# Optimization experiments

Measured on AMD Instinct MI355X. Metric: run time of the kernel, lower is better.

## Reference

```python
import jax, jax.numpy as jnp
import numpy as np

H = 16          # n_heads
DH = 128        # head_dim
DR = 64         # rope_dim
DC = DH - DR    # content_dim = 64
THETA = 10000.0
SCALE = 1.0 / np.sqrt(DH)


def _rope_tables(T, dtype):
    inv = 1.0 / (THETA ** (jnp.arange(0, DR, 2, dtype=jnp.float32) / DR))  # [DR/2]
    t = jnp.arange(T, dtype=jnp.float32)
    freqs = jnp.outer(t, inv)  # [T, DR/2]
    return jnp.cos(freqs).astype(dtype), jnp.sin(freqs).astype(dtype)


def _apply_rope(x, cos, sin):
    # x: [B,H,T,DR]; cos/sin: [T,DR/2] broadcast over B,H
    d = x.shape[-1] // 2
    x1, x2 = x[..., :d], x[..., d:]
    return jnp.concatenate([x1 * cos - x2 * sin, x1 * sin + x2 * cos], axis=-1)


def setup_inputs() -> dict:
    key = jax.random.key(0)
    ks = jax.random.split(key, 9)
    B, T, D = 1, 2048, 2048
    s = 0.02
    return {
        "x": jax.random.normal(ks[0], (B, T, D), jnp.float32),
        "Wq_down": jax.random.normal(ks[1], (D, 512), jnp.float32) * s,
        "Wq_up": jax.random.normal(ks[2], (512, H * DC), jnp.float32) * s,
        "Wq_rope": jax.random.normal(ks[3], (D, H * DR), jnp.float32) * s,
        "Wkv_down": jax.random.normal(ks[4], (D, 512), jnp.float32) * s,
        "Wk_up": jax.random.normal(ks[5], (512, H * DC), jnp.float32) * s,
        "Wv_up": jax.random.normal(ks[6], (512, H * DH), jnp.float32) * s,
        "Wk_rope": jax.random.normal(ks[7], (D, H * DR), jnp.float32) * s,
        "Wo": jax.random.normal(ks[8], (H * DH, D), jnp.float32) * s,
    }


def reference(x, Wq_down, Wq_up, Wq_rope, Wkv_down, Wk_up, Wv_up, Wk_rope, Wo):
    B, T, D = x.shape
    # low-rank query path: down then up, content part only
    q_content = ((x @ Wq_down) @ Wq_up).reshape(B, T, H, DC).transpose(0, 2, 1, 3)
    q_pos = (x @ Wq_rope).reshape(B, T, H, DR).transpose(0, 2, 1, 3)
    kv_latent = x @ Wkv_down                    # [B,T,d_latent]
    k_pos = (x @ Wk_rope).reshape(B, T, H, DR).transpose(0, 2, 1, 3)

    cos, sin = _rope_tables(T, x.dtype)
    q_pos = _apply_rope(q_pos, cos, sin)
    k_pos = _apply_rope(k_pos, cos, sin)

    k_content = (kv_latent @ Wk_up).reshape(B, T, H, DC).transpose(0, 2, 1, 3)
    v = (kv_latent @ Wv_up).reshape(B, T, H, DH).transpose(0, 2, 1, 3)

    q = jnp.concatenate([q_content, q_pos], axis=-1)  # [B,H,T,DH]
    k = jnp.concatenate([k_content, k_pos], axis=-1)  # [B,H,T,DH]

    scores = jnp.einsum("bhtd,bhsd->bhts", q, k) * SCALE
    causal = jnp.tril(jnp.ones((T, T), dtype=bool))
    scores = jnp.where(causal, scores, jnp.finfo(scores.dtype).min)
    attn = jax.nn.softmax(scores, axis=-1)
    out = jnp.einsum("bhts,bhsd->bhtd", attn, v)       # [B,H,T,DH]
    out = out.transpose(0, 2, 1, 3).reshape(B, T, H * DH)
    return out @ Wo
```

## Files before the change

### kernel.cpp

```cpp
#include <hip/hip_runtime.h>
#include <math.h>

#define T_SEQ 2048
#define D_MODEL 2048
#define H_HEADS 16
#define DH 128
#define DR 64
#define DC 64
#define D_LAT 512
#define SEGLEN 7
#define NSEG_TOT 46
#define NSEG_OF(q) ((2 * (q) + 2 + SEGLEN - 1) / SEGLEN)
#define QSCALE (0.08838834764831845f * 1.4426950408889634f)

typedef __attribute__((ext_vector_type(8))) short short8;
typedef __attribute__((ext_vector_type(4))) short short4v;
typedef __attribute__((ext_vector_type(4))) float f32x4;

#if __has_builtin(__builtin_amdgcn_exp2f)
#define EXP2(x) __builtin_amdgcn_exp2f(x)
#else
#define EXP2(x) exp2f(x)
#endif

__device__ __forceinline__ float bf2f(short b) {
    unsigned u = ((unsigned)(unsigned short)b) << 16;
    return __builtin_bit_cast(float, u);
}
__device__ __forceinline__ short f2bf(float f) {
    unsigned u = __builtin_bit_cast(unsigned, f);
    unsigned r = u + 0x7fffu + ((u >> 16) & 1u);
    return (short)(r >> 16);
}
__device__ __forceinline__ unsigned f2bf_tru(float f) {
    return __builtin_bit_cast(unsigned, f) >> 16;
}

#define GLD_LDS(gp, lp) \
    __builtin_amdgcn_global_load_lds( \
        (const __attribute__((address_space(1))) void*)(gp), \
        (__attribute__((address_space(3))) void*)(lp), 16, 0, 0)

__device__ __forceinline__ void ct_tile(float (*tile)[33],
                                        const float* __restrict__ W,
                                        short* __restrict__ Wt,
                                        int R, int C, int ldo, int rel) {
    int bx = rel % (C / 32), by = rel / (C / 32);
    int c0 = bx * 32, r0 = by * 32;
    int tx = threadIdx.x & 31, ty = threadIdx.x >> 5;
    #pragma unroll
    for (int i = 0; i < 4; ++i)
        tile[ty + i * 8][tx] = W[(size_t)(r0 + ty + i * 8) * C + c0 + tx];
    __syncthreads();
    #pragma unroll
    for (int i = 0; i < 4; ++i)
        Wt[(size_t)(c0 + ty + i * 8) * ldo + r0 + tx] = f2bf(tile[tx][ty + i * 8]);
    __syncthreads();
}

__global__ __launch_bounds__(256) void prep(const float* __restrict__ x,
                                            short* __restrict__ xb,
                                            const float* __restrict__ Wqd,
                                            const float* __restrict__ Wkvd,
                                            const float* __restrict__ Wqr,
                                            const float* __restrict__ Wkr,
                                            const float* __restrict__ Wqu,
                                            const float* __restrict__ Wku,
                                            const float* __restrict__ Wvu,
                                            const float* __restrict__ Wo,
                                            short* __restrict__ WdT,
                                            short* __restrict__ WupT2,
                                            short* __restrict__ WoT) {
    __shared__ float tile[32][33];
    int bid = blockIdx.x;
    if (bid < 4096) {
        int i = bid * 1024 + threadIdx.x * 4;
        float4 f = *(const float4*)&x[i];
        short4v o;
        o.x = f2bf(f.x); o.y = f2bf(f.y); o.z = f2bf(f.z); o.w = f2bf(f.w);
        *(short4v*)&xb[i] = o;
    } else if (bid < 5120) {
        ct_tile(tile, Wqd,  WdT + (size_t)0 * 2048,    2048, 512,  2048, bid - 4096);
    } else if (bid < 6144) {
        ct_tile(tile, Wkvd, WdT + (size_t)512 * 2048,  2048, 512,  2048, bid - 5120);
    } else if (bid < 8192) {
        ct_tile(tile, Wqr,  WdT + (size_t)1024 * 2048, 2048, 1024, 2048, bid - 6144);
    } else if (bid < 10240) {
        ct_tile(tile, Wkr,  WdT + (size_t)2048 * 2048, 2048, 1024, 2048, bid - 8192);
    } else if (bid < 10752) {
        ct_tile(tile, Wqu,  WupT2 + (size_t)0 * 512,    512, 1024, 512, bid - 10240);
    } else if (bid < 11264) {
        ct_tile(tile, Wku,  WupT2 + (size_t)1024 * 512, 512, 1024, 512, bid - 10752);
    } else if (bid < 12288) {
        ct_tile(tile, Wvu,  WupT2 + (size_t)2048 * 512, 512, 2048, 512, bid - 11264);
    } else {
        ct_tile(tile, Wo,   WoT, 2048, 2048, 2048, bid - 12288);
    }
}

__global__ __launch_bounds__(256) void transpose_bf16(const short* __restrict__ in,
                                                      short* __restrict__ vTc,
                                                      int ldi) {
    __shared__ short tile[64][65];
    int c0 = blockIdx.x * 64, t0 = blockIdx.y * 64;
    int tx = threadIdx.x & 31, ty = threadIdx.x >> 5;
    #pragma unroll
    for (int i = 0; i < 8; ++i) {
        int r = ty + i * 8;
        int vv = *(const int*)&in[(size_t)(t0 + r) * ldi + c0 + tx * 2];
        tile[r][tx * 2]     = (short)(vv & 0xffff);
        tile[r][tx * 2 + 1] = (short)(((unsigned)vv) >> 16);
    }
    __syncthreads();
    #pragma unroll
    for (int i = 0; i < 8; ++i) {
        int G = i * 256 + threadIdx.x;
        int ch2 = G >> 10;
        int rem = G & 1023;
        int dl = rem >> 4;
        int mp = rem & 15;
        int dval = c0 + dl;
        int h = dval >> 7, d128 = dval & 127;
        int kl = 4 * ((mp >> 2) ^ (d128 & 3)) + (mp & 3);
        unsigned lo = (unsigned short)tile[ch2 * 32 + kl][dl];
        unsigned hi = (unsigned short)tile[ch2 * 32 + kl + 16][dl];
        int chg = (t0 >> 5) + ch2;
        size_t off = ((size_t)(h * 64 + chg)) * 4096 + d128 * 32 + mp * 2;
        *(int*)&vTc[off] = (int)(lo | (hi << 16));
    }
}

__global__ __launch_bounds__(256) void gemm_bt(const short* __restrict__ A,
                                               const short* __restrict__ A2,
                                               const short* __restrict__ Bt,
                                               short* __restrict__ C0,
                                               short* __restrict__ C1,
                                               short* __restrict__ C2,
                                               short* __restrict__ C3,
                                               int N, int Kblk,
                                               int lda, int ldb, int ldc,
                                               int ncut, int scut, float cscale) {
    __shared__ short As[128 * 64];
    __shared__ short Bs[128 * 64];
    const int tid = threadIdx.x;
    const int wave = tid >> 6, lane = tid & 63;
    const int lin = blockIdx.x;
    const int X = N >> 7, Xq = X >> 2;
    const int xcd = lin & 7;
    int r = lin >> 3;
    const int bx = (xcd & 3) * Xq + (r % Xq); r /= Xq;
    const int by = (xcd >> 2) * 8 + (r & 7);
    const int bz = r >> 3;
    const int row0 = by * 128, col0 = bx * 128;
    const int kbase = bz * Kblk;
    const short* Ause = (col0 < ncut) ? A : A2;
    short* Cuse = (bz == 0) ? C0 : (bz == 1) ? C1 : (bz == 2) ? C2 : C3;
    const int wr = (wave >> 1) * 64, wc = (wave & 1) * 64;
    const int lr = lane & 15, quad = lane >> 4;

    f32x4 acc[4][4];
    #pragma unroll
    for (int i = 0; i < 4; ++i)
        #pragma unroll
        for (int j = 0; j < 4; ++j) acc[i][j] = (f32x4){0.f, 0.f, 0.f, 0.f};

    for (int k0 = kbase; k0 < kbase + Kblk; k0 += 64) {
        __syncthreads();
        #pragma unroll
        for (int it = 0; it < 4; ++it) {
            int idx = wave * 64 + it * 256 + lane;
            int row = idx >> 3;
            int scg = (idx & 7) ^ (row & 7);
            const short* ga = Ause + (size_t)(row0 + row) * lda + k0 + scg * 8;
            const short* gb = Bt   + (size_t)(col0 + row) * ldb + k0 + scg * 8;
            int lds0 = (wave * 64 + it * 256) * 8;
            GLD_LDS(ga, &As[lds0]);
            GLD_LDS(gb, &Bs[lds0]);
        }
        __syncthreads();

        #pragma unroll
        for (int kk = 0; kk < 2; ++kk) {
            short8 af[4], bfr[4];
            #pragma unroll
            for (int i = 0; i < 4; ++i)
                af[i] = *(const short8*)
                    &As[(wr + i * 16 + lr) * 64 + (((kk * 4 + quad) ^ (lr & 7)) * 8)];
            #pragma unroll
            for (int j = 0; j < 4; ++j)
                bfr[j] = *(const short8*)
                    &Bs[(wc + j * 16 + lr) * 64 + (((kk * 4 + quad) ^ (lr & 7)) * 8)];
            #pragma unroll
            for (int i = 0; i < 4; ++i)
                #pragma unroll
                for (int j = 0; j < 4; ++j)
                    acc[i][j] = __builtin_amdgcn_mfma_f32_16x16x32_bf16(
                        af[i], bfr[j], acc[i][j], 0, 0, 0);
        }
    }

    const float sc = (col0 < scut) ? cscale : 1.0f;
    #pragma unroll
    for (int i = 0; i < 4; ++i) {
        int rb = row0 + wr + i * 16 + quad * 4;
        #pragma unroll
        for (int j = 0; j < 4; ++j) {
            int c = col0 + wc + j * 16 + lr;
            #pragma unroll
            for (int rr = 0; rr < 4; ++rr)
                Cuse[(size_t)(rb + rr) * ldc + c] = f2bf(acc[i][j][rr] * sc);
        }
    }
}

__global__ __launch_bounds__(192) void finish_down(short* __restrict__ cat,
                                                   const short* __restrict__ pdown) {
    const int t = blockIdx.x;
    const int k8 = threadIdx.x * 8;
    const int c0 = ((k8 >> 5) << 6) + (k8 & 31);
    const size_t lo = (size_t)t * 3072 + c0;
    const size_t hi = lo + 32;
    short8 al = *(const short8*)&cat[lo];
    short8 ah = *(const short8*)&cat[hi];
    short8 bl = *(const short8*)&pdown[lo];
    short8 bh = *(const short8*)&pdown[hi];
    float xl[8], xh[8];
    #pragma unroll
    for (int j = 0; j < 8; ++j) {
        xl[j] = bf2f(al[j]) + bf2f(bl[j]);
        xh[j] = bf2f(ah[j]) + bf2f(bh[j]);
    }
    if (c0 >= 1024) {
        float sc = (c0 < 2048) ? QSCALE : 1.0f;
        #pragma unroll
        for (int j = 0; j < 8; ++j) {
            int i = (c0 & 31) + j;
            float freq = (float)t * __powf(10000.0f, -(float)i / 32.0f);
            float cs = __cosf(freq), sn = __sinf(freq);
            float r1 = (xl[j] * cs - xh[j] * sn) * sc;
            float r2 = (xl[j] * sn + xh[j] * cs) * sc;
            xl[j] = r1; xh[j] = r2;
        }
    }
    short8 ol, oh;
    #pragma unroll
    for (int j = 0; j < 8; ++j) { ol[j] = f2bf(xl[j]); oh[j] = f2bf(xh[j]); }
    *(short8*)&cat[lo] = ol;
    *(short8*)&cat[hi] = oh;
}

__global__ __launch_bounds__(256) void add_out_f32(const short* __restrict__ p0,
                                                   const short* __restrict__ p1,
                                                   float* __restrict__ out) {
    int i = (blockIdx.x * 256 + threadIdx.x) * 4;
    short4v a = *(const short4v*)&p0[i];
    short4v b = *(const short4v*)&p1[i];
    float4 o;
    o.x = bf2f(a.x) + bf2f(b.x);
    o.y = bf2f(a.y) + bf2f(b.y);
    o.z = bf2f(a.z) + bf2f(b.z);
    o.w = bf2f(a.w) + bf2f(b.w);
    *(float4*)&out[i] = o;
}

__global__ __launch_bounds__(256) void attn_mla_split(const short* __restrict__ qkup,
                                                      const short* __restrict__ cat,
                                                      const short* __restrict__ vTc,
                                                      short* __restrict__ slabA,
                                                      short* __restrict__ slabB,
                                                      float* __restrict__ lpart) {
    const int lin = blockIdx.x;
    const int xcd = lin & 7;
    int k_ = lin >> 3;
    const int h = xcd + 8 * (k_ & 1);
    const int pp = k_ >> 1;
    int qt = 0, s = 0, acc = 0;
    #pragma unroll
    for (int q = 0; q < 16; ++q) {
        const int ns = NSEG_OF(q);
        if (pp >= acc) { qt = q; s = pp - acc; }
        acc += ns;
    }
    const int nchunk = 2 * qt + 2;
    const int nsq = NSEG_OF(qt);
    const int cbase = nchunk / nsq, crem = nchunk % nsq;
    const int c0 = s * cbase + (s < crem ? s : crem);
    const int c1 = c0 + cbase + (s < crem ? 1 : 0);

    const int tid = threadIdx.x;
    const int wave = tid >> 6, lane = tid & 63;
    const int lr = lane & 15, quad = lane >> 4;

    __shared__ short Ks[2][32 * 128];
    __shared__ short Vst[2][128 * 32];
    __shared__ short Ps[4][2][16 * 40];

    const short8 ones = {0x3F80, 0x3F80, 0x3F80, 0x3F80,
                         0x3F80, 0x3F80, 0x3F80, 0x3F80};

    const int Q0 = qt * 128;
    const int qrowA = Q0 + wave * 16;
    const int qrowB = qrowA + 64;

    short8 qf[2][4];
    #pragma unroll
    for (int sb = 0; sb < 2; ++sb) {
        int t = (sb ? qrowB : qrowA) + lr;
        #pragma unroll
        for (int kci = 0; kci < 4; ++kci) {
            const short* src = (kci < 2)
                ? qkup + (size_t)t * 4096 + h * 64
                : cat + (size_t)t * 3072 + 1024 + h * 64;
            qf[sb][kci] = *(const short8*)&src[(kci & 1) * 32 + quad * 8];
        }
    }

    const int idx = wave * 64 + lane;
    const int key = idx >> 4;
    const int cg = (idx & 15) ^ (key & 15);
    const short* kp0 = (cg < 8)
        ? qkup + (size_t)key * 4096 + 1024 + h * 64 + cg * 8
        : cat + (size_t)key * 3072 + 2048 + h * 64 + (cg - 8) * 8;
    const int kst = (cg < 8) ? 4096 : 3072;
    const short* kp1 = kp0 + (size_t)16 * kst;
    const short* vp0 = vTc + ((size_t)h * 64 + (size_t)c0 * 2) * 4096 + idx * 8;
    kp0 += (size_t)c0 * 64 * kst; kp1 += (size_t)c0 * 64 * kst;
    const int kadv = 64 * kst;
    const int kph = 32 * kst;
    const int ldsA = (wave * 64) * 8;
    const int ldsB = (wave * 64 + 256) * 8;

    f32x4 Oacc[2][8];
    #pragma unroll
    for (int sb = 0; sb < 2; ++sb)
        #pragma unroll
        for (int d = 0; d < 8; ++d) Oacc[sb][d] = (f32x4){0.f, 0.f, 0.f, 0.f};
    f32x4 Lacc[2];
    Lacc[0] = (f32x4){0.f, 0.f, 0.f, 0.f};
    Lacc[1] = (f32x4){0.f, 0.f, 0.f, 0.f};

    for (int cc = c0; cc < c1; ++cc) {
        __syncthreads();
        GLD_LDS(kp0,        &Ks[0][ldsA]);
        GLD_LDS(kp1,        &Ks[0][ldsB]);
        GLD_LDS(kp0 + kph,  &Ks[1][ldsA]);
        GLD_LDS(kp1 + kph,  &Ks[1][ldsB]);
        GLD_LDS(vp0,        &Vst[0][ldsA]);
        GLD_LDS(vp0 + 2048, &Vst[0][ldsB]);
        GLD_LDS(vp0 + 4096, &Vst[1][ldsA]);
        GLD_LDS(vp0 + 6144, &Vst[1][ldsB]);
        kp0 += kadv; kp1 += kadv; vp0 += 8192;
        __syncthreads();

        #pragma unroll
        for (int half = 0; half < 2; ++half) {
            const int s0 = cc * 64 + half * 32;
            if (s0 > qrowB + 15) continue;
            const bool actA = (s0 <= qrowA + 15);
            const short* Kc = Ks[half];
            const short* Vc = Vst[half];

            f32x4 sacc[2][2];
            #pragma unroll
            for (int sb = 0; sb < 2; ++sb)
                #pragma unroll
                for (int n = 0; n < 2; ++n) sacc[sb][n] = (f32x4){0.f, 0.f, 0.f, 0.f};
            #pragma unroll
            for (int n = 0; n < 2; ++n) {
                #pragma unroll
                for (int kci = 0; kci < 4; ++kci) {
                    short8 kf = *(const short8*)
                        &Kc[(n * 16 + lr) * 128 + ((kci * 4 + quad) ^ lr) * 8];
                    if (actA)
                        sacc[0][n] = __builtin_amdgcn_mfma_f32_16x16x32_bf16(
                            qf[0][kci], kf, sacc[0][n], 0, 0, 0);
                    sacc[1][n] = __builtin_amdgcn_mfma_f32_16x16x32_bf16(
                        qf[1][kci], kf, sacc[1][n], 0, 0, 0);
                }
            }
            #pragma unroll
            for (int sb = 0; sb < 2; ++sb) {
                if (sb == 0 && !actA) continue;
                const int qrow0 = sb ? qrowB : qrowA;
                if (s0 + 31 > qrow0) {
                    #pragma unroll
                    for (int r = 0; r < 4; ++r) {
                        int qg = qrow0 + quad * 4 + r;
                        #pragma unroll
                        for (int n = 0; n < 2; ++n) {
                            int sidx = s0 + n * 16 + lr;
                            sacc[sb][n][r] = (sidx <= qg) ? sacc[sb][n][r] : -1e30f;
                        }
                    }
                }
                #pragma unroll
                for (int r = 0; r < 4; ++r) {
                    unsigned pk = f2bf_tru(EXP2(sacc[sb][0][r])) |
                                  (f2bf_tru(EXP2(sacc[sb][1][r])) << 16);
                    *(unsigned*)&Ps[wave][sb][(quad * 4 + r) * 40 + lr * 2] = pk;
                }
            }
            short8 pfA, pfB;
            if (actA) {
                pfA = *(const short8*)&Ps[wave][0][lr * 40 + quad * 8];
                Lacc[0] = __builtin_amdgcn_mfma_f32_16x16x32_bf16(pfA, ones,
                                                                  Lacc[0], 0, 0, 0);
            }
            pfB = *(const short8*)&Ps[wave][1][lr * 40 + quad * 8];
            Lacc[1] = __builtin_amdgcn_mfma_f32_16x16x32_bf16(pfB, ones,
                                                              Lacc[1], 0, 0, 0);
            #pragma unroll
            for (int dt = 0; dt < 8; ++dt) {
                short8 vf = *(const short8*)
                    &Vc[(dt * 16 + lr) * 32 + (quad ^ (lr & 3)) * 8];
                if (actA)
                    Oacc[0][dt] = __builtin_amdgcn_mfma_f32_16x16x32_bf16(
                        pfA, vf, Oacc[0][dt], 0, 0, 0);
                Oacc[1][dt] = __builtin_amdgcn_mfma_f32_16x16x32_bf16(
                    pfB, vf, Oacc[1][dt], 0, 0, 0);
            }
        }
    }

    const int slot = h * NSEG_TOT + pp;
    short* slotp = (slot < 512) ? slabA + (size_t)slot * 16384
                                : slabB + (size_t)(slot - 512) * 16384;
    #pragma unroll
    for (int sb = 0; sb < 2; ++sb) {
        const int rbase = wave * 16 + sb * 64 + quad * 4;
        #pragma unroll
        for (int r = 0; r < 4; ++r) {
            #pragma unroll
            for (int dt = 0; dt < 8; ++dt)
                slotp[(rbase + r) * 128 + dt * 16 + lr] = f2bf(Oacc[sb][dt][r]);
        }
        if (lr == 0) {
            #pragma unroll
            for (int r = 0; r < 4; ++r)
                lpart[(size_t)slot * 128 + rbase + r] = Lacc[sb][r];
        }
    }
}

__global__ __launch_bounds__(256) void attn_combine(const short* __restrict__ slabA,
                                                    const short* __restrict__ slabB,
                                                    const float* __restrict__ lpart,
                                                    short* __restrict__ ao) {
    const int t = blockIdx.x;
    const int qt = t >> 7, rl = t & 127;
    const int h = threadIdx.x >> 4;
    const int di = (threadIdx.x & 15) * 8;
    int pf = 0;
    #pragma unroll
    for (int q = 0; q < 16; ++q)
        if (q < qt) pf += NSEG_OF(q);
    const int ns = NSEG_OF(qt);
    float o[8] = {0.f, 0.f, 0.f, 0.f, 0.f, 0.f, 0.f, 0.f};
    float den = 0.f;
    for (int s = 0; s < ns; ++s) {
        const int slot = h * NSEG_TOT + pf + s;
        const short* sp = (slot < 512) ? slabA + (size_t)slot * 16384
                                       : slabB + (size_t)(slot - 512) * 16384;
        short8 v = *(const short8*)&sp[rl * 128 + di];
        #pragma unroll
        for (int j = 0; j < 8; ++j) o[j] += bf2f(v[j]);
        den += lpart[(size_t)slot * 128 + rl];
    }
    float inv = 1.0f / den;
    short8 ov;
    #pragma unroll
    for (int j = 0; j < 8; ++j) ov[j] = f2bf(o[j] * inv);
    *(short8*)&ao[(size_t)t * 2048 + h * 128 + di] = ov;
}

extern "C" void kernel_launch(void* const* d_in, const int* in_sizes, int n_in,
                              void* d_out, int out_size, void* d_ws, size_t ws_size,
                              hipStream_t stream) {
    const float* x        = (const float*)d_in[0];
    const float* Wq_down  = (const float*)d_in[1];
    const float* Wq_up    = (const float*)d_in[2];
    const float* Wq_rope  = (const float*)d_in[3];
    const float* Wkv_down = (const float*)d_in[4];
    const float* Wk_up    = (const float*)d_in[5];
    const float* Wv_up    = (const float*)d_in[6];
    const float* Wk_rope  = (const float*)d_in[7];
    const float* Wo       = (const float*)d_in[8];
    float* out = (float*)d_out;

    short* p = (short*)d_ws;
    short* xb     = p; p += (size_t)2048 * 2048;
    short* WoT    = p; p += (size_t)2048 * 2048;
    short* cat    = p; p += (size_t)2048 * 3072;
    short* upcat2 = p; p += (size_t)2048 * 4096;
    short* WdT    = p; p += (size_t)3072 * 2048;
    short* WupT2  = p; p += (size_t)4096 * 512;
    short* vTc    = p; p += (size_t)2048 * 2048;
    float* lpart  = (float*)p;
    short* pdown   = upcat2;
    short* aob     = cat;
    short* slabA   = WdT;
    short* slabB   = xb;
    short* pw0     = upcat2;
    short* pw1     = upcat2 + (size_t)2048 * 2048;

    prep<<<dim3(16384), 256, 0, stream>>>(x, xb, Wq_down, Wkv_down, Wq_rope,
                                          Wk_rope, Wq_up, Wk_up, Wv_up, Wo,
                                          WdT, WupT2, WoT);

    gemm_bt<<<dim3(24 * 16 * 2), 256, 0, stream>>>(xb, xb, WdT, cat, pdown,
                                                   nullptr, nullptr,
                                                   3072, 1024,
                                                   2048, 2048, 3072, 1 << 30, 0, 1.f);

    finish_down<<<dim3(2048), 192, 0, stream>>>(cat, pdown);

    gemm_bt<<<dim3(32 * 16 * 1), 256, 0, stream>>>(cat, cat + 512, WupT2,
                                                   upcat2, nullptr, nullptr, nullptr,
                                                   4096, 512,
                                                   3072, 512, 4096, 1024, 1024, QSCALE);

    transpose_bf16<<<dim3(32, 32), 256, 0, stream>>>(upcat2 + 2048, vTc, 4096);

    attn_mla_split<<<dim3(16 * NSEG_TOT), 256, 0, stream>>>(upcat2, cat, vTc,
                                                            slabA, slabB, lpart);
    attn_combine<<<dim3(2048), 256, 0, stream>>>(slabA, slabB, lpart, aob);

    gemm_bt<<<dim3(16 * 16 * 2), 256, 0, stream>>>(aob, aob, WoT, pw0, pw1,
                                                   nullptr, nullptr,
                                                   2048, 1024,
                                                   2048, 2048, 2048, 1 << 30, 0, 1.f);
    add_out_f32<<<dim3(2048 * 2048 / 1024), 256, 0, stream>>>(pw0, pw1, out);
}
```

Measured before the change: 261.6 us.

## Compute transposed scores so P stays in registers, dropping LDS round-trip

The QK^T MFMA operands are swapped so each lane holds the scores for one query row across consecutive keys. The exponentiated probabilities can then be packed straight into the A-operand of the PV MFMA, with no write to and read back from shared memory. The V transpose kernel's k-ordering is changed to match the new per-lane key permutation, and the causal mask is re-indexed for the transposed layout. This removes an LDS store/load and its latency from the attention inner loop, but correctness depends on the permuted V layout matching the MFMA register layout exactly.

```diff
diff --git a/kernel.cpp b/kernel.cpp
--- a/kernel.cpp
+++ b/kernel.cpp
@@ -121,9 +121,11 @@
         int mp = rem & 15;
         int dval = c0 + dl;
         int h = dval >> 7, d128 = dval & 127;
-        int kl = 4 * ((mp >> 2) ^ (d128 & 3)) + (mp & 3);
+        int g  = (mp >> 2) ^ (d128 & 3);
+        int mi = mp & 3;
+        int kl = 4 * g + 2 * (mi & 1) + 16 * (mi >> 1);
         unsigned lo = (unsigned short)tile[ch2 * 32 + kl][dl];
-        unsigned hi = (unsigned short)tile[ch2 * 32 + kl + 16][dl];
+        unsigned hi = (unsigned short)tile[ch2 * 32 + kl + 1][dl];
         int chg = (t0 >> 5) + ch2;
         size_t off = ((size_t)(h * 64 + chg)) * 4096 + d128 * 32 + mp * 2;
         *(int*)&vTc[off] = (int)(lo | (hi << 16));
@@ -293,7 +295,6 @@
 
     __shared__ short Ks[2][32 * 128];
     __shared__ short Vst[2][128 * 32];
-    __shared__ short Ps[4][2][16 * 40];
 
     const short8 ones = {0x3F80, 0x3F80, 0x3F80, 0x3F80,
                          0x3F80, 0x3F80, 0x3F80, 0x3F80};
@@ -373,41 +374,43 @@
                         &Kc[(n * 16 + lr) * 128 + ((kci * 4 + quad) ^ lr) * 8];
                     if (actA)
                         sacc[0][n] = __builtin_amdgcn_mfma_f32_16x16x32_bf16(
-                            qf[0][kci], kf, sacc[0][n], 0, 0, 0);
+                            kf, qf[0][kci], sacc[0][n], 0, 0, 0);
                     sacc[1][n] = __builtin_amdgcn_mfma_f32_16x16x32_bf16(
-                        qf[1][kci], kf, sacc[1][n], 0, 0, 0);
+                        kf, qf[1][kci], sacc[1][n], 0, 0, 0);
                 }
             }
+            short8 paA, paB;
             #pragma unroll
             for (int sb = 0; sb < 2; ++sb) {
                 if (sb == 0 && !actA) continue;
                 const int qrow0 = sb ? qrowB : qrowA;
                 if (s0 + 31 > qrow0) {
                     #pragma unroll
-                    for (int r = 0; r < 4; ++r) {
-                        int qg = qrow0 + quad * 4 + r;
+                    for (int n = 0; n < 2; ++n) {
                         #pragma unroll
-                        for (int n = 0; n < 2; ++n) {
-                            int sidx = s0 + n * 16 + lr;
-                            sacc[sb][n][r] = (sidx <= qg) ? sacc[sb][n][r] : -1e30f;
+                        for (int r = 0; r < 4; ++r) {
+                            int kidx = s0 + n * 16 + quad * 4 + r;
+                            sacc[sb][n][r] = (kidx <= qrow0 + lr)
+                                           ? sacc[sb][n][r] : -1e30f;
                         }
                     }
                 }
-                #pragma unroll
-                for (int r = 0; r < 4; ++r) {
-                    unsigned pk = f2bf_tru(EXP2(sacc[sb][0][r])) |
-                                  (f2bf_tru(EXP2(sacc[sb][1][r])) << 16);
-                    *(unsigned*)&Ps[wave][sb][(quad * 4 + r) * 40 + lr * 2] = pk;
-                }
+                int4 pw;
+                pw.x = (int)(f2bf_tru(EXP2(sacc[sb][0][0])) |
+                             (f2bf_tru(EXP2(sacc[sb][0][1])) << 16));
+                pw.y = (int)(f2bf_tru(EXP2(sacc[sb][0][2])) |
+                             (f2bf_tru(EXP2(sacc[sb][0][3])) << 16));
+                pw.z = (int)(f2bf_tru(EXP2(sacc[sb][1][0])) |
+                             (f2bf_tru(EXP2(sacc[sb][1][1])) << 16));
+                pw.w = (int)(f2bf_tru(EXP2(sacc[sb][1][2])) |
+                             (f2bf_tru(EXP2(sacc[sb][1][3])) << 16));
+                if (sb) paB = __builtin_bit_cast(short8, pw);
+                else    paA = __builtin_bit_cast(short8, pw);
             }
-            short8 pfA, pfB;
-            if (actA) {
-                pfA = *(const short8*)&Ps[wave][0][lr * 40 + quad * 8];
-                Lacc[0] = __builtin_amdgcn_mfma_f32_16x16x32_bf16(pfA, ones,
+            if (actA)
+                Lacc[0] = __builtin_amdgcn_mfma_f32_16x16x32_bf16(paA, ones,
                                                                   Lacc[0], 0, 0, 0);
-            }
-            pfB = *(const short8*)&Ps[wave][1][lr * 40 + quad * 8];
-            Lacc[1] = __builtin_amdgcn_mfma_f32_16x16x32_bf16(pfB, ones,
+            Lacc[1] = __builtin_amdgcn_mfma_f32_16x16x32_bf16(paB, ones,
                                                               Lacc[1], 0, 0, 0);
             #pragma unroll
             for (int dt = 0; dt < 8; ++dt) {
@@ -415,9 +418,9 @@
                     &Vc[(dt * 16 + lr) * 32 + (quad ^ (lr & 3)) * 8];
                 if (actA)
                     Oacc[0][dt] = __builtin_amdgcn_mfma_f32_16x16x32_bf16(
-                        pfA, vf, Oacc[0][dt], 0, 0, 0);
+                        paA, vf, Oacc[0][dt], 0, 0, 0);
                 Oacc[1][dt] = __builtin_amdgcn_mfma_f32_16x16x32_bf16(
-                    pfB, vf, Oacc[1][dt], 0, 0, 0);
+                    paB, vf, Oacc[1][dt], 0, 0, 0);
             }
         }
     }
```

Result: no change. 257.7 us (-1.5%).
